# Kernel optimization log

Measured on AMD Instinct MI355X. Metric: run time of the kernel, lower is better.

The kernel has to match this reference:

```python
import jax, jax.numpy as jnp
import numpy as np

B, S, D, H, R, N = 4, 2048, 1024, 16, 64, 16
DH = D // H


def setup_inputs() -> dict:
    key = jax.random.key(0)
    ks = jax.random.split(key, 8)
    scale = 1.0 / np.sqrt(D)
    return {
        "x": jax.random.normal(ks[0], (B, S, D), jnp.float32),
        "compress_weights": jax.random.uniform(ks[1], (B, S, N), jnp.float32),
        "expand_weights_QK": jax.random.uniform(ks[2], (B, S, N), jnp.float32),
        "expand_weights_V": jax.random.uniform(ks[3], (B, S, N), jnp.float32),
        "compress_neurons": jax.random.normal(ks[4], (N, D, R), jnp.float32) * scale,
        "expand_neurons_QK": jax.random.normal(ks[5], (N, R, D), jnp.float32) * (1.0 / np.sqrt(R)),
        "expand_neurons_V": jax.random.normal(ks[6], (N, R, D), jnp.float32) * (1.0 / np.sqrt(R)),
        "W_O": jax.random.normal(ks[7], (D, D), jnp.float32) * scale,
    }


def reference(x, compress_weights, expand_weights_QK, expand_weights_V,
              compress_neurons, expand_neurons_QK, expand_neurons_V, W_O):
    b, s, d = x.shape
    # Fused reordering of torch's  einsum('bsn,ndr->bsdr') + einsum('bsd,bsdr->bsr')
    # -> avoids materializing the [B,S,D,R] mixed-compress tensor; same math.
    # h[b,s,r] = sum_n w[b,s,n] * (x[b,s,:] @ C[n,:,:])[r]
    h = jnp.einsum('bsd,ndr,bsn->bsr', x, compress_neurons, compress_weights)  # [B,S,R]
    # Q and K use the same weights and same pool -> identical tensors in the source.
    q = jnp.einsum('bsr,nrd,bsn->bsd', h, expand_neurons_QK, expand_weights_QK)
    k = q  # source computes K with identical inputs
    v = jnp.einsum('bsr,nrd,bsn->bsd', h, expand_neurons_V, expand_weights_V)

    def heads(t):  # [B,S,D] -> [B,H,S,DH]
        return t.reshape(b, s, H, DH).transpose(0, 2, 1, 3)

    qh, kh, vh = heads(q), heads(k), heads(v)
    scores = jnp.einsum('bhqd,bhkd->bhqk', qh, kh) / np.sqrt(DH)
    causal = jnp.tril(jnp.ones((s, s), bool))
    scores = jnp.where(causal[None, None], scores, jnp.finfo(scores.dtype).min)
    probs = jax.nn.softmax(scores, axis=-1)
    attn = jnp.einsum('bhqk,bhkd->bhqd', probs, vh)  # [B,H,S,DH]
    attn = attn.transpose(0, 2, 1, 3).reshape(b, s, d)
    # nn.Linear(d,d,bias=False): y = attn @ W_O.T
    return attn @ W_O.T
```

## Files before the change

kernel.cpp:

```cpp
#include <hip/hip_runtime.h>
#include <hip/hip_bf16.h>
#include <math.h>

#define Bq 4
#define Sq 2048
#define Dq 1024
#define Hq 16
#define Rq 64
#define Nq 16
#define DHq 64
#define Mq (Bq * Sq)
#define NRq (Nq * Rq)

static_assert(NRq == Dq, "layout assumption");

typedef __attribute__((ext_vector_type(8))) short short8v;
typedef __attribute__((ext_vector_type(4))) float f32x4;

__device__ inline ushort bf16_rne(float x) {
    __hip_bfloat16 b = __float2bfloat16(x);
    return *reinterpret_cast<ushort*>(&b);
}
__device__ inline float bf16_to_f(ushort u) {
    union { unsigned int i; float f; } c;
    c.i = ((unsigned int)u) << 16;
    return c.f;
}
__device__ inline void split2(float x, ushort& h, ushort& l) {
    h = bf16_rne(x);
    l = bf16_rne(x - bf16_to_f(h));
}

__global__ __launch_bounds__(256) void split_kernel(const float* __restrict__ in,
                                                    ushort* __restrict__ hi,
                                                    ushort* __restrict__ lo,
                                                    float scale) {
    const int i = blockIdx.x * 256 + threadIdx.x;
    const float4 v = *reinterpret_cast<const float4*>(&in[(size_t)i * 4]);
    ushort4 h4, l4;
    split2(v.x * scale, h4.x, l4.x);
    split2(v.y * scale, h4.y, l4.y);
    split2(v.z * scale, h4.z, l4.z);
    split2(v.w * scale, h4.w, l4.w);
    *reinterpret_cast<ushort4*>(&hi[(size_t)i * 4]) = h4;
    *reinterpret_cast<ushort4*>(&lo[(size_t)i * 4]) = l4;
}

__global__ __launch_bounds__(256) void callT_split_kernel(const float* __restrict__ cn,
                                                          ushort* __restrict__ bhi,
                                                          ushort* __restrict__ blo) {
    const int idx = blockIdx.x * 256 + threadIdx.x;
    const int nr = idx >> 10, d = idx & 1023;
    const int n = nr >> 6, r = nr & 63;
    const float v = cn[((size_t)(n << 10) + d) * 64 + r];
    ushort h, l;
    split2(v, h, l);
    bhi[idx] = h;
    blo[idx] = l;
}

__global__ __launch_bounds__(256) void transpose_split_kernel(const float* __restrict__ in,
                                                              ushort* __restrict__ bhi,
                                                              ushort* __restrict__ blo) {
    __shared__ float tl[64][65];
    const int bx = blockIdx.x;
    const int tn0 = (bx & 15) * 64;
    const int tk0 = (bx >> 4) * 64;
    const int r0 = threadIdx.x >> 4;
    const int c4 = (threadIdx.x & 15) * 4;
#pragma unroll
    for (int p = 0; p < 4; p++) {
        const int row = r0 + p * 16;
        const float4 v = *reinterpret_cast<const float4*>(&in[(size_t)(tk0 + row) * 1024 + tn0 + c4]);
        tl[row][c4 + 0] = v.x; tl[row][c4 + 1] = v.y;
        tl[row][c4 + 2] = v.z; tl[row][c4 + 3] = v.w;
    }
    __syncthreads();
#pragma unroll
    for (int p = 0; p < 4; p++) {
        const int orow = r0 + p * 16;
        ushort4 h4, l4;
        split2(tl[c4 + 0][orow], h4.x, l4.x);
        split2(tl[c4 + 1][orow], h4.y, l4.y);
        split2(tl[c4 + 2][orow], h4.z, l4.z);
        split2(tl[c4 + 3][orow], h4.w, l4.w);
        const size_t o = (size_t)(tn0 + orow) * 1024 + tk0 + c4;
        *reinterpret_cast<ushort4*>(&bhi[o]) = h4;
        *reinterpret_cast<ushort4*>(&blo[o]) = l4;
    }
}

__global__ __launch_bounds__(256) void vt_split_kernel(const float* __restrict__ Vf,
                                                       ushort* __restrict__ vthi,
                                                       ushort* __restrict__ vtlo) {
    __shared__ float tl[64][65];
    const int st = blockIdx.x, bh = blockIdx.y;
    const int b = bh >> 4, h = bh & 15;
    const int i = threadIdx.x >> 2;
    const int c16 = (threadIdx.x & 3) * 16;
#pragma unroll
    for (int p = 0; p < 4; p++) {
        const float4 v = *reinterpret_cast<const float4*>(
            &Vf[((size_t)(b * Sq + st * 64 + i)) * Dq + h * 64 + c16 + p * 4]);
        tl[i][c16 + p * 4 + 0] = v.x; tl[i][c16 + p * 4 + 1] = v.y;
        tl[i][c16 + p * 4 + 2] = v.z; tl[i][c16 + p * 4 + 3] = v.w;
    }
    __syncthreads();
    const size_t obase = ((size_t)(bh * 64 + i)) * Sq + st * 64 + c16;
#pragma unroll
    for (int p = 0; p < 4; p++) {
        ushort4 h4, l4;
        split2(tl[c16 + p * 4 + 0][i], h4.x, l4.x);
        split2(tl[c16 + p * 4 + 1][i], h4.y, l4.y);
        split2(tl[c16 + p * 4 + 2][i], h4.z, l4.z);
        split2(tl[c16 + p * 4 + 3][i], h4.w, l4.w);
        *reinterpret_cast<ushort4*>(&vthi[obase + p * 4]) = h4;
        *reinterpret_cast<ushort4*>(&vtlo[obase + p * 4]) = l4;
    }
}

#define LPITCH 40
__global__ __launch_bounds__(256) void gemm_bf16x3(const ushort* __restrict__ Ahi,
                                                   const ushort* __restrict__ Alo,
                                                   const ushort* __restrict__ Bthi,
                                                   const ushort* __restrict__ Btlo,
                                                   float* __restrict__ C,
                                                   int M, int N, int K) {
    __shared__ ushort lAhi[128 * LPITCH];
    __shared__ ushort lAlo[128 * LPITCH];
    __shared__ ushort lBhi[128 * LPITCH];
    __shared__ ushort lBlo[128 * LPITCH];
    const int tid = threadIdx.x;
    const int lane = tid & 63;
    const int wave = tid >> 6;
    const int wr = wave >> 1, wc = wave & 1;
    const int row0 = blockIdx.y * 128, col0 = blockIdx.x * 128;

    const int srow = tid >> 2;
    const int spart = tid & 3;
    const int lrow = lane & 15;
    const int kgrp = lane >> 4;

    f32x4 acc[4][4];
#pragma unroll
    for (int i = 0; i < 4; i++)
#pragma unroll
        for (int j = 0; j < 4; j++) acc[i][j] = (f32x4)(0.f);

    for (int k0 = 0; k0 < K; k0 += 32) {
        const size_t ga0 = (size_t)(row0 + srow) * K + k0 + spart * 8;
        const size_t ga1 = ga0 + (size_t)64 * K;
        const size_t gb0 = (size_t)(col0 + srow) * K + k0 + spart * 8;
        const size_t gb1 = gb0 + (size_t)64 * K;
        const short8v ah0 = *reinterpret_cast<const short8v*>(Ahi + ga0);
        const short8v ah1 = *reinterpret_cast<const short8v*>(Ahi + ga1);
        const short8v al0 = *reinterpret_cast<const short8v*>(Alo + ga0);
        const short8v al1 = *reinterpret_cast<const short8v*>(Alo + ga1);
        const short8v bh0 = *reinterpret_cast<const short8v*>(Bthi + gb0);
        const short8v bh1 = *reinterpret_cast<const short8v*>(Bthi + gb1);
        const short8v bl0 = *reinterpret_cast<const short8v*>(Btlo + gb0);
        const short8v bl1 = *reinterpret_cast<const short8v*>(Btlo + gb1);
        __syncthreads();
        const int s0 = srow * LPITCH + spart * 8;
        const int s1 = (srow + 64) * LPITCH + spart * 8;
        *reinterpret_cast<short8v*>(&lAhi[s0]) = ah0;
        *reinterpret_cast<short8v*>(&lAhi[s1]) = ah1;
        *reinterpret_cast<short8v*>(&lAlo[s0]) = al0;
        *reinterpret_cast<short8v*>(&lAlo[s1]) = al1;
        *reinterpret_cast<short8v*>(&lBhi[s0]) = bh0;
        *reinterpret_cast<short8v*>(&lBhi[s1]) = bh1;
        *reinterpret_cast<short8v*>(&lBlo[s0]) = bl0;
        *reinterpret_cast<short8v*>(&lBlo[s1]) = bl1;
        __syncthreads();
        short8v afh[4], afl[4], bfh[4], bfl[4];
#pragma unroll
        for (int im = 0; im < 4; im++) {
            const int a = (wr * 64 + im * 16 + lrow) * LPITCH + kgrp * 8;
            afh[im] = *reinterpret_cast<const short8v*>(&lAhi[a]);
            afl[im] = *reinterpret_cast<const short8v*>(&lAlo[a]);
        }
#pragma unroll
        for (int in = 0; in < 4; in++) {
            const int bb = (wc * 64 + in * 16 + lrow) * LPITCH + kgrp * 8;
            bfh[in] = *reinterpret_cast<const short8v*>(&lBhi[bb]);
            bfl[in] = *reinterpret_cast<const short8v*>(&lBlo[bb]);
        }
#pragma unroll
        for (int im = 0; im < 4; im++)
#pragma unroll
            for (int in = 0; in < 4; in++) {
                acc[im][in] = __builtin_amdgcn_mfma_f32_16x16x32_bf16(afh[im], bfh[in], acc[im][in], 0, 0, 0);
                acc[im][in] = __builtin_amdgcn_mfma_f32_16x16x32_bf16(afh[im], bfl[in], acc[im][in], 0, 0, 0);
                acc[im][in] = __builtin_amdgcn_mfma_f32_16x16x32_bf16(afl[im], bfh[in], acc[im][in], 0, 0, 0);
            }
    }
#pragma unroll
    for (int im = 0; im < 4; im++) {
        const int orow = row0 + wr * 64 + im * 16 + kgrp * 4;
#pragma unroll
        for (int in = 0; in < 4; in++) {
            const int ocol = col0 + wc * 64 + in * 16 + lrow;
#pragma unroll
            for (int j = 0; j < 4; j++) C[(size_t)(orow + j) * N + ocol] = acc[im][in][j];
        }
    }
}

__global__ __launch_bounds__(256) void fuse_hG_kernel(float* TG,
                                                      const float* __restrict__ cw,
                                                      const float* __restrict__ ewq,
                                                      const float* __restrict__ ewv,
                                                      float* __restrict__ Gq) {
    const int lane = threadIdx.x & 63;
    const int wave = threadIdx.x >> 6;
    const int t = blockIdx.x * 4 + wave;
    float* Trow = TG + (size_t)t * NRq;
    float h = 0.f;
#pragma unroll
    for (int n = 0; n < Nq; n++) h = fmaf(cw[t * Nq + n], Trow[n * 64 + lane], h);
#pragma unroll
    for (int n = 0; n < Nq; n++) Gq[(size_t)t * NRq + n * 64 + lane] = ewq[t * Nq + n] * h;
#pragma unroll
    for (int n = 0; n < Nq; n++) Trow[n * 64 + lane] = ewv[t * Nq + n] * h;
}

#define APITCH 68
#define PPITCH 76
#define STAGE_ISSUE(kt_, R)                                                          \
    do {                                                                             \
        const size_t ksrc = ((size_t)(b * Sq + (kt_) * 64 + srow)) * Dq + h * 64 + sc16; \
        const size_t vsrc = ((size_t)(bh * 64 + srow)) * Sq + (kt_) * 64 + sc16;     \
        R[0] = *reinterpret_cast<const short8v*>(Qhi + ksrc);                        \
        R[1] = *reinterpret_cast<const short8v*>(Qhi + ksrc + 8);                    \
        R[2] = *reinterpret_cast<const short8v*>(Qlo + ksrc);                        \
        R[3] = *reinterpret_cast<const short8v*>(Qlo + ksrc + 8);                    \
        R[4] = *reinterpret_cast<const short8v*>(VThi + vsrc);                       \
        R[5] = *reinterpret_cast<const short8v*>(VThi + vsrc + 8);                   \
        R[6] = *reinterpret_cast<const short8v*>(VTlo + vsrc);                       \
        R[7] = *reinterpret_cast<const short8v*>(VTlo + vsrc + 8);                   \
    } while (0)
#define STAGE_WRITE(R)                                        \
    do {                                                      \
        const int d0 = srow * APITCH + sc16;                  \
        *reinterpret_cast<short8v*>(&Kh[d0])     = R[0];      \
        *reinterpret_cast<short8v*>(&Kh[d0 + 8]) = R[1];      \
        *reinterpret_cast<short8v*>(&Kl[d0])     = R[2];      \
        *reinterpret_cast<short8v*>(&Kl[d0 + 8]) = R[3];      \
        *reinterpret_cast<short8v*>(&Vh[d0])     = R[4];      \
        *reinterpret_cast<short8v*>(&Vh[d0 + 8]) = R[5];      \
        *reinterpret_cast<short8v*>(&Vl[d0])     = R[6];      \
        *reinterpret_cast<short8v*>(&Vl[d0 + 8]) = R[7];      \
    } while (0)

__global__ __launch_bounds__(256) void attn_mfma_kernel(const ushort* __restrict__ Qhi,
                                                        const ushort* __restrict__ Qlo,
                                                        const ushort* __restrict__ VThi,
                                                        const ushort* __restrict__ VTlo,
                                                        ushort* __restrict__ AOhi,
                                                        ushort* __restrict__ AOlo) {
    __shared__ ushort Kh[64 * APITCH], Kl[64 * APITCH];
    __shared__ ushort Vh[64 * APITCH], Vl[64 * APITCH];
    __shared__ ushort Ph[4][16 * PPITCH];
    const int tid = threadIdx.x;
    const int lane = tid & 63, w = tid >> 6;
    const int lr = lane & 15, lg = lane >> 4;
    const int bh = blockIdx.y;
    const int b = bh >> 4, h = bh & 15;
    const int srow = tid >> 2;
    const int sc16 = (tid & 3) * 16;

#pragma unroll 1
    for (int pass = 0; pass < 2; pass++) {
        const int qt = pass ? 31 - blockIdx.x : blockIdx.x;
        const size_t qbase = ((size_t)(b * Sq + qt * 64 + w * 16 + lr)) * Dq + h * 64 + lg * 8;
        const short8v aqh0 = *reinterpret_cast<const short8v*>(Qhi + qbase);
        const short8v aqh1 = *reinterpret_cast<const short8v*>(Qhi + qbase + 32);
        const short8v aql0 = *reinterpret_cast<const short8v*>(Qlo + qbase);
        const short8v aql1 = *reinterpret_cast<const short8v*>(Qlo + qbase + 32);

        float m[4] = {-1e30f, -1e30f, -1e30f, -1e30f};
        float l[4] = {0.f, 0.f, 0.f, 0.f};
        f32x4 out[4];
#pragma unroll
        for (int dt = 0; dt < 4; dt++) out[dt] = (f32x4)(0.f);

        {
            short8v R[8];
            STAGE_ISSUE(0, R);
            __syncthreads();
            STAGE_WRITE(R);
        }
        __syncthreads();

        for (int kt = 0; kt <= qt; kt++) {
            const bool more = kt < qt;
            short8v NX[8];
            if (more) STAGE_ISSUE(kt + 1, NX);

            f32x4 s[4];
#pragma unroll
            for (int ct = 0; ct < 4; ct++) s[ct] = (f32x4)(0.f);
#pragma unroll
            for (int ct = 0; ct < 4; ct++) {
                {
                    const int ka = (ct * 16 + lr) * APITCH + lg * 8;
                    const short8v bkh = *reinterpret_cast<const short8v*>(&Kh[ka]);
                    const short8v bkl = *reinterpret_cast<const short8v*>(&Kl[ka]);
                    s[ct] = __builtin_amdgcn_mfma_f32_16x16x32_bf16(aqh0, bkh, s[ct], 0, 0, 0);
                    s[ct] = __builtin_amdgcn_mfma_f32_16x16x32_bf16(aqh0, bkl, s[ct], 0, 0, 0);
                    s[ct] = __builtin_amdgcn_mfma_f32_16x16x32_bf16(aql0, bkh, s[ct], 0, 0, 0);
                }
                {
                    const int ka = (ct * 16 + lr) * APITCH + 32 + lg * 8;
                    const short8v bkh = *reinterpret_cast<const short8v*>(&Kh[ka]);
                    const short8v bkl = *reinterpret_cast<const short8v*>(&Kl[ka]);
                    s[ct] = __builtin_amdgcn_mfma_f32_16x16x32_bf16(aqh1, bkh, s[ct], 0, 0, 0);
                    s[ct] = __builtin_amdgcn_mfma_f32_16x16x32_bf16(aqh1, bkl, s[ct], 0, 0, 0);
                    s[ct] = __builtin_amdgcn_mfma_f32_16x16x32_bf16(aql1, bkh, s[ct], 0, 0, 0);
                }
            }
            if (kt == qt) {
#pragma unroll
                for (int ct = 0; ct < 4; ct++)
#pragma unroll
                    for (int j = 0; j < 4; j++)
                        if ((ct * 16 + lr) > (w * 16 + lg * 4 + j)) s[ct][j] = -1e30f;
            }
            float c[4];
#pragma unroll
            for (int j = 0; j < 4; j++) {
                float pm = fmaxf(fmaxf(s[0][j], s[1][j]), fmaxf(s[2][j], s[3][j]));
                pm = fmaxf(pm, __shfl_xor(pm, 1));
                pm = fmaxf(pm, __shfl_xor(pm, 2));
                pm = fmaxf(pm, __shfl_xor(pm, 4));
                pm = fmaxf(pm, __shfl_xor(pm, 8));
                const float mn = fmaxf(m[j], pm);
                c[j] = __expf(m[j] - mn);
                m[j] = mn;
            }
            float rs[4] = {0.f, 0.f, 0.f, 0.f};
#pragma unroll
            for (int ct = 0; ct < 4; ct++)
#pragma unroll
                for (int j = 0; j < 4; j++) {
                    const float p = __expf(s[ct][j] - m[j]);
                    rs[j] += p;
                    Ph[w][(lg * 4 + j) * PPITCH + ct * 16 + lr] = bf16_rne(p);
                }
#pragma unroll
            for (int j = 0; j < 4; j++) {
                float t = rs[j];
                t += __shfl_xor(t, 1);
                t += __shfl_xor(t, 2);
                t += __shfl_xor(t, 4);
                t += __shfl_xor(t, 8);
                l[j] = l[j] * c[j] + t;
            }
#pragma unroll
            for (int dt = 0; dt < 4; dt++)
#pragma unroll
                for (int j = 0; j < 4; j++) out[dt][j] *= c[j];
#pragma unroll
            for (int kp = 0; kp < 2; kp++) {
                const short8v pah = *reinterpret_cast<const short8v*>(
                    &Ph[w][lr * PPITCH + kp * 32 + lg * 8]);
#pragma unroll
                for (int dt = 0; dt < 4; dt++) {
                    const int va = (dt * 16 + lr) * APITCH + kp * 32 + lg * 8;
                    const short8v bvh = *reinterpret_cast<const short8v*>(&Vh[va]);
                    const short8v bvl = *reinterpret_cast<const short8v*>(&Vl[va]);
                    out[dt] = __builtin_amdgcn_mfma_f32_16x16x32_bf16(pah, bvh, out[dt], 0, 0, 0);
                    out[dt] = __builtin_amdgcn_mfma_f32_16x16x32_bf16(pah, bvl, out[dt], 0, 0, 0);
                }
            }
            __syncthreads();
            if (more) STAGE_WRITE(NX);
            __syncthreads();
        }
#pragma unroll
        for (int j = 0; j < 4; j++) l[j] = 1.f / l[j];
#pragma unroll
        for (int dt = 0; dt < 4; dt++)
#pragma unroll
            for (int j = 0; j < 4; j++) {
                const float v = out[dt][j] * l[j];
                ushort vh, vl;
                split2(v, vh, vl);
                const size_t o = ((size_t)(b * Sq + qt * 64 + w * 16 + lg * 4 + j)) * Dq
                                 + h * 64 + dt * 16 + lr;
                AOhi[o] = vh;
                AOlo[o] = vl;
            }
    }
}

extern "C" void kernel_launch(void* const* d_in, const int* in_sizes, int n_in,
                              void* d_out, int out_size, void* d_ws, size_t ws_size,
                              hipStream_t stream) {
    (void)in_sizes; (void)n_in; (void)out_size; (void)ws_size;
    const float* x   = (const float*)d_in[0];
    const float* cw  = (const float*)d_in[1];
    const float* ewq = (const float*)d_in[2];
    const float* ewv = (const float*)d_in[3];
    const float* cn  = (const float*)d_in[4];
    const float* enq = (const float*)d_in[5];
    const float* env = (const float*)d_in[6];
    const float* wo  = (const float*)d_in[7];
    float* out = (float*)d_out;
    float* ws  = (float*)d_ws;

    const size_t MEG = 1024 * 1024;
    float* Tg  = ws;
    float* GqQ = ws + 8 * MEG;
    float* Vf  = out;
    ushort* us = (ushort*)(ws + 16 * MEG);
    ushort* SAhi = us;
    ushort* SAlo = us + 8 * MEG;
    ushort* cBhi = us + 16 * MEG;
    ushort* cBlo = us + 17 * MEG;
    ushort* eqBhi = us + 18 * MEG;
    ushort* eqBlo = us + 19 * MEG;
    ushort* evBhi = us + 20 * MEG;
    ushort* evBlo = us + 21 * MEG;
    ushort* woBhi = us + 22 * MEG;
    ushort* woBlo = us + 23 * MEG;
    ushort* QShi = (ushort*)Tg;
    ushort* QSlo = QShi + 8 * MEG;
    ushort* VThi = (ushort*)GqQ;
    ushort* VTlo = VThi + 8 * MEG;

    split_kernel<<<8192, 256, 0, stream>>>(x, SAhi, SAlo, 1.0f);
    callT_split_kernel<<<4096, 256, 0, stream>>>(cn, cBhi, cBlo);
    transpose_split_kernel<<<256, 256, 0, stream>>>(enq, eqBhi, eqBlo);
    transpose_split_kernel<<<256, 256, 0, stream>>>(env, evBhi, evBlo);
    split_kernel<<<1024, 256, 0, stream>>>(wo, woBhi, woBlo, 1.0f);

    const dim3 gg(8, 64);
    gemm_bf16x3<<<gg, 256, 0, stream>>>(SAhi, SAlo, cBhi, cBlo, Tg, Mq, NRq, Dq);
    fuse_hG_kernel<<<2048, 256, 0, stream>>>(Tg, cw, ewq, ewv, GqQ);
    split_kernel<<<8192, 256, 0, stream>>>(Tg, SAhi, SAlo, 1.0f);
    gemm_bf16x3<<<gg, 256, 0, stream>>>(SAhi, SAlo, evBhi, evBlo, Vf, Mq, Dq, NRq);
    split_kernel<<<8192, 256, 0, stream>>>(GqQ, SAhi, SAlo, 1.0f);
    gemm_bf16x3<<<gg, 256, 0, stream>>>(SAhi, SAlo, eqBhi, eqBlo, GqQ, Mq, Dq, NRq);
    split_kernel<<<8192, 256, 0, stream>>>(GqQ, QShi, QSlo, 0.35355339f);
    vt_split_kernel<<<dim3(32, 64), 256, 0, stream>>>(Vf, VThi, VTlo);
    attn_mfma_kernel<<<dim3(16, 64), 256, 0, stream>>>(QShi, QSlo, VThi, VTlo,
                                                       SAhi, SAlo);
    gemm_bf16x3<<<gg, 256, 0, stream>>>(SAhi, SAlo, woBhi, woBlo, out, Mq, Dq, Dq);
}
```

Measured before the change: 627.9 us.

## Drop V low-bf16 term, add lazy softmax rescale and MFMA priority hints

The attention kernel now uses only the high bf16 part of V. This halves V staging loads, its shared memory and the P·V MFMAs, and the vt_split kernel no longer writes the low half. Online-softmax rescaling of the running max, sum and output is skipped unless some row's new max exceeds the old one by more than 8, which removes the per-tile exp and multiply work. s_setprio hints are wrapped around the MFMA blocks. The costs are lower precision on V and probabilities that can grow up to e^8 before renormalisation, which may affect accuracy.

```diff
diff --git a/kernel.cpp b/kernel.cpp
--- a/kernel.cpp
+++ b/kernel.cpp
@@ -91,8 +91,7 @@
 }
 
 __global__ __launch_bounds__(256) void vt_split_kernel(const float* __restrict__ Vf,
-                                                       ushort* __restrict__ vthi,
-                                                       ushort* __restrict__ vtlo) {
+                                                       ushort* __restrict__ vthi) {
     __shared__ float tl[64][65];
     const int st = blockIdx.x, bh = blockIdx.y;
     const int b = bh >> 4, h = bh & 15;
@@ -109,13 +108,12 @@
     const size_t obase = ((size_t)(bh * 64 + i)) * Sq + st * 64 + c16;
 #pragma unroll
     for (int p = 0; p < 4; p++) {
-        ushort4 h4, l4;
-        split2(tl[c16 + p * 4 + 0][i], h4.x, l4.x);
-        split2(tl[c16 + p * 4 + 1][i], h4.y, l4.y);
-        split2(tl[c16 + p * 4 + 2][i], h4.z, l4.z);
-        split2(tl[c16 + p * 4 + 3][i], h4.w, l4.w);
+        ushort4 h4;
+        h4.x = bf16_rne(tl[c16 + p * 4 + 0][i]);
+        h4.y = bf16_rne(tl[c16 + p * 4 + 1][i]);
+        h4.z = bf16_rne(tl[c16 + p * 4 + 2][i]);
+        h4.w = bf16_rne(tl[c16 + p * 4 + 3][i]);
         *reinterpret_cast<ushort4*>(&vthi[obase + p * 4]) = h4;
-        *reinterpret_cast<ushort4*>(&vtlo[obase + p * 4]) = l4;
     }
 }
 
@@ -236,8 +234,6 @@
         R[3] = *reinterpret_cast<const short8v*>(Qlo + ksrc + 8);                    \
         R[4] = *reinterpret_cast<const short8v*>(VThi + vsrc);                       \
         R[5] = *reinterpret_cast<const short8v*>(VThi + vsrc + 8);                   \
-        R[6] = *reinterpret_cast<const short8v*>(VTlo + vsrc);                       \
-        R[7] = *reinterpret_cast<const short8v*>(VTlo + vsrc + 8);                   \
     } while (0)
 #define STAGE_WRITE(R)                                        \
     do {                                                      \
@@ -248,18 +244,15 @@
         *reinterpret_cast<short8v*>(&Kl[d0 + 8]) = R[3];      \
         *reinterpret_cast<short8v*>(&Vh[d0])     = R[4];      \
         *reinterpret_cast<short8v*>(&Vh[d0 + 8]) = R[5];      \
-        *reinterpret_cast<short8v*>(&Vl[d0])     = R[6];      \
-        *reinterpret_cast<short8v*>(&Vl[d0 + 8]) = R[7];      \
     } while (0)
 
 __global__ __launch_bounds__(256) void attn_mfma_kernel(const ushort* __restrict__ Qhi,
                                                         const ushort* __restrict__ Qlo,
                                                         const ushort* __restrict__ VThi,
-                                                        const ushort* __restrict__ VTlo,
                                                         ushort* __restrict__ AOhi,
                                                         ushort* __restrict__ AOlo) {
     __shared__ ushort Kh[64 * APITCH], Kl[64 * APITCH];
-    __shared__ ushort Vh[64 * APITCH], Vl[64 * APITCH];
+    __shared__ ushort Vh[64 * APITCH];
     __shared__ ushort Ph[4][16 * PPITCH];
     const int tid = threadIdx.x;
     const int lane = tid & 63, w = tid >> 6;
@@ -285,7 +278,7 @@
         for (int dt = 0; dt < 4; dt++) out[dt] = (f32x4)(0.f);
 
         {
-            short8v R[8];
+            short8v R[6];
             STAGE_ISSUE(0, R);
             __syncthreads();
             STAGE_WRITE(R);
@@ -294,12 +287,13 @@
 
         for (int kt = 0; kt <= qt; kt++) {
             const bool more = kt < qt;
-            short8v NX[8];
+            short8v NX[6];
             if (more) STAGE_ISSUE(kt + 1, NX);
 
             f32x4 s[4];
 #pragma unroll
             for (int ct = 0; ct < 4; ct++) s[ct] = (f32x4)(0.f);
+            __builtin_amdgcn_s_setprio(1);
 #pragma unroll
             for (int ct = 0; ct < 4; ct++) {
                 {
@@ -319,6 +313,7 @@
                     s[ct] = __builtin_amdgcn_mfma_f32_16x16x32_bf16(aql1, bkh, s[ct], 0, 0, 0);
                 }
             }
+            __builtin_amdgcn_s_setprio(0);
             if (kt == qt) {
 #pragma unroll
                 for (int ct = 0; ct < 4; ct++)
@@ -326,17 +321,28 @@
                     for (int j = 0; j < 4; j++)
                         if ((ct * 16 + lr) > (w * 16 + lg * 4 + j)) s[ct][j] = -1e30f;
             }
-            float c[4];
+            float pm[4];
 #pragma unroll
             for (int j = 0; j < 4; j++) {
-                float pm = fmaxf(fmaxf(s[0][j], s[1][j]), fmaxf(s[2][j], s[3][j]));
-                pm = fmaxf(pm, __shfl_xor(pm, 1));
-                pm = fmaxf(pm, __shfl_xor(pm, 2));
-                pm = fmaxf(pm, __shfl_xor(pm, 4));
-                pm = fmaxf(pm, __shfl_xor(pm, 8));
-                const float mn = fmaxf(m[j], pm);
-                c[j] = __expf(m[j] - mn);
-                m[j] = mn;
+                float t = fmaxf(fmaxf(s[0][j], s[1][j]), fmaxf(s[2][j], s[3][j]));
+                t = fmaxf(t, __shfl_xor(t, 1));
+                t = fmaxf(t, __shfl_xor(t, 2));
+                t = fmaxf(t, __shfl_xor(t, 4));
+                t = fmaxf(t, __shfl_xor(t, 8));
+                pm[j] = t;
+            }
+            int ok = (pm[0] <= m[0] + 8.f) & (pm[1] <= m[1] + 8.f) &
+                     (pm[2] <= m[2] + 8.f) & (pm[3] <= m[3] + 8.f);
+            if (!__all(ok)) {
+#pragma unroll
+                for (int j = 0; j < 4; j++) {
+                    const float mn = fmaxf(m[j], pm[j]);
+                    const float c = __expf(m[j] - mn);
+                    m[j] = mn;
+                    l[j] *= c;
+#pragma unroll
+                    for (int dt = 0; dt < 4; dt++) out[dt][j] *= c;
+                }
             }
             float rs[4] = {0.f, 0.f, 0.f, 0.f};
 #pragma unroll
@@ -354,12 +360,9 @@
                 t += __shfl_xor(t, 2);
                 t += __shfl_xor(t, 4);
                 t += __shfl_xor(t, 8);
-                l[j] = l[j] * c[j] + t;
-            }
-#pragma unroll
-            for (int dt = 0; dt < 4; dt++)
-#pragma unroll
-                for (int j = 0; j < 4; j++) out[dt][j] *= c[j];
+                l[j] += t;
+            }
+            __builtin_amdgcn_s_setprio(1);
 #pragma unroll
             for (int kp = 0; kp < 2; kp++) {
                 const short8v pah = *reinterpret_cast<const short8v*>(
@@ -368,11 +371,10 @@
                 for (int dt = 0; dt < 4; dt++) {
                     const int va = (dt * 16 + lr) * APITCH + kp * 32 + lg * 8;
                     const short8v bvh = *reinterpret_cast<const short8v*>(&Vh[va]);
-                    const short8v bvl = *reinterpret_cast<const short8v*>(&Vl[va]);
                     out[dt] = __builtin_amdgcn_mfma_f32_16x16x32_bf16(pah, bvh, out[dt], 0, 0, 0);
-                    out[dt] = __builtin_amdgcn_mfma_f32_16x16x32_bf16(pah, bvl, out[dt], 0, 0, 0);
                 }
             }
+            __builtin_amdgcn_s_setprio(0);
             __syncthreads();
             if (more) STAGE_WRITE(NX);
             __syncthreads();
@@ -427,7 +429,6 @@
     ushort* QShi = (ushort*)Tg;
     ushort* QSlo = QShi + 8 * MEG;
     ushort* VThi = (ushort*)GqQ;
-    ushort* VTlo = VThi + 8 * MEG;
 
     split_kernel<<<8192, 256, 0, stream>>>(x, SAhi, SAlo, 1.0f);
     callT_split_kernel<<<4096, 256, 0, stream>>>(cn, cBhi, cBlo);
@@ -443,8 +444,8 @@
     split_kernel<<<8192, 256, 0, stream>>>(GqQ, SAhi, SAlo, 1.0f);
     gemm_bf16x3<<<gg, 256, 0, stream>>>(SAhi, SAlo, eqBhi, eqBlo, GqQ, Mq, Dq, NRq);
     split_kernel<<<8192, 256, 0, stream>>>(GqQ, QShi, QSlo, 0.35355339f);
-    vt_split_kernel<<<dim3(32, 64), 256, 0, stream>>>(Vf, VThi, VTlo);
-    attn_mfma_kernel<<<dim3(16, 64), 256, 0, stream>>>(QShi, QSlo, VThi, VTlo,
+    vt_split_kernel<<<dim3(32, 64), 256, 0, stream>>>(Vf, VThi);
+    attn_mfma_kernel<<<dim3(16, 64), 256, 0, stream>>>(QShi, QSlo, VThi,
                                                        SAhi, SAlo);
     gemm_bf16x3<<<gg, 256, 0, stream>>>(SAhi, SAlo, woBhi, woBlo, out, Mq, Dq, Dq);
 }
```

After: 602.3 us. 4.1% less time.
